# Optimization experiments

Measured on AMD Instinct MI355X. Metric: run time of the kernel, lower is better.

## Reference

```python
import jax, jax.numpy as jnp
import numpy as np

CHANNEL = 1
ALPHA = 1.0
EPS = 1e-10
SHAPE = (1, CHANNEL, 160, 192, 160)


def _sobel_kernels(channel):
    s2 = np.array([[-1., 0., 1.], [-2., 0., 2.], [-1., 0., 1.]], dtype=np.float32)
    # sobel.repeat(channel,1,3,1,1): 2D kernel tiled along depth -> k[d,h,w] = s2[h,w]
    kx = np.tile(s2[None, :, :], (3, 1, 1))
    ky = np.tile(s2.T[None, :, :], (3, 1, 1))
    kz = np.array([[[-1., -1., -1.], [-2., -2., -2.], [-1., -1., -1.]],
                   [[0., 0., 0.], [0., 0., 0.], [0., 0., 0.]],
                   [[1., 1., 1.], [2., 2., 2.], [1., 1., 1.]]], dtype=np.float32)
    def rep(k):  # -> [channel, 1, 3, 3, 3] for depthwise conv
        return jnp.asarray(np.tile(k[None, None], (channel, 1, 1, 1, 1)))
    return rep(kx), rep(ky), rep(kz)


def _conv3d(x, k, channel):
    # torch F.conv3d (cross-correlation), padding=1, groups=channel
    return jax.lax.conv_general_dilated(
        x, k, window_strides=(1, 1, 1), padding=((1, 1), (1, 1), (1, 1)),
        dimension_numbers=('NCDHW', 'OIDHW', 'NCDHW'),
        feature_group_count=channel)


def setup_inputs() -> dict:
    key = jax.random.key(0)
    k1, k2, k3 = jax.random.split(key, 3)
    M = jax.random.normal(k1, SHAPE, dtype=jnp.float32)
    S = jax.random.normal(k2, SHAPE, dtype=jnp.float32)
    flow = jax.random.normal(k3, (SHAPE[0], 3) + SHAPE[2:], dtype=jnp.float32)
    return {"M": M, "S": S, "flow": flow}


def reference(M, S, flow):
    kx, ky, kz = _sobel_kernels(CHANNEL)
    Idiff = M - S
    Sx = _conv3d(S, kx, CHANNEL)
    Sy = _conv3d(S, ky, CHANNEL)
    Sz = _conv3d(S, kz, CHANNEL)
    Mx = _conv3d(M, kx, CHANNEL)
    My = _conv3d(M, ky, CHANNEL)
    Mz = _conv3d(M, kz, CHANNEL)
    Sxyz_mag = Sx ** 2 + Sy ** 2 + Sz ** 2
    Mxyz_mag = Mx ** 2 + My ** 2 + Mz ** 2
    denom_S = Sxyz_mag + (ALPHA ** 2) * Idiff ** 2 + 1e-10
    denom_M = Mxyz_mag + (ALPHA ** 2) * Idiff ** 2 + 1e-10
    Ux = Idiff * (Sx / denom_S + Mx / denom_M)
    Uy = Idiff * (Sy / denom_S + My / denom_M)
    Uz = Idiff * (Sz / denom_S + Mz / denom_M)
    demons_ori_xz = jnp.arctan(Ux / (Uz + EPS))
    demons_ori_yz = jnp.arctan(Uy / (Uz + EPS))
    flow_ori_xz = jnp.arctan(flow[:, 0] / (flow[:, 2] + EPS))
    flow_ori_yz = jnp.arctan(flow[:, 1] / (flow[:, 2] + EPS))
    ori_error = jnp.mean((flow_ori_xz - demons_ori_xz) ** 2) + \
                jnp.mean((flow_ori_yz - demons_ori_yz) ** 2)
    return ori_error
```

## Files before the change

### kernel.cpp

```cpp
#include <hip/hip_runtime.h>
#include <math.h>

#define DD 160
#define HH 192
#define WW 160
#define TW 32
#define TH 8
#define TD 8
#define HW (HH * WW)
#define NVOX (DD * HH * WW)
#define HTW (TW + 2)
#define HTH (TH + 2)
#define HALO (HTW * HTH)

__device__ __forceinline__ float atan_fast(float r) {
    float ar = fabsf(r);
    float inv = __builtin_amdgcn_rcpf(ar);
    bool big = ar > 1.0f;
    float x = big ? inv : ar;
    float x2 = x * x;
    float p = fmaf(x2, fmaf(x2, fmaf(x2, fmaf(x2, fmaf(x2,
              -0.0117212f, 0.05265332f), -0.11643287f), 0.19354346f),
              -0.33262347f), 0.99997726f);
    p *= x;
    float res = big ? (1.57079632679489662f - p) : p;
    return copysignf(res, r);
}

__global__ __launch_bounds__(256) void demons_ori_kernel(
    const float* __restrict__ Mv, const float* __restrict__ Sv,
    const float* __restrict__ flow, float* __restrict__ out)
{
    __shared__ float buf[2][2][HTH][HTW];
    __shared__ float redbuf[4];

    const int tid = threadIdx.x;
    const int tw = tid & 31;
    const int th = tid >> 5;
    const int w0 = blockIdx.x * TW;
    const int h0 = blockIdx.y * TH;
    const int d0 = blockIdx.z * TD;

    int nst = 0;
    int sidx[2];
    int gbase[2];
    bool gok[2];
    for (int i = tid; i < HALO; i += 256) {
        int hh = i / HTW, ww = i - hh * HTW;
        int gh = h0 + hh - 1, gw = w0 + ww - 1;
        sidx[nst] = i;
        gok[nst] = (gh >= 0 && gh < HH && gw >= 0 && gw < WW);
        gbase[nst] = gh * WW + gw;
        nst++;
    }

    const int hc = th + 1, wc = tw + 1;

    auto stage = [&](int d, float pq[2][4]) {
        float* __restrict__ bS = &buf[d & 1][0][0][0];
        float* __restrict__ bM = &buf[d & 1][1][0][0];
        const bool din = (d >= 0) && (d < DD);
        for (int j = 0; j < nst; ++j) {
            float vs = 0.f, vm = 0.f;
            if (din && gok[j]) {
                size_t off = (size_t)d * HW + gbase[j];
                vs = Sv[off];
                vm = Mv[off];
            }
            bS[sidx[j]] = vs;
            bM[sidx[j]] = vm;
        }
        __syncthreads();
        #pragma unroll
        for (int f = 0; f < 2; ++f) {
            const float* __restrict__ b = f ? bM : bS;
            const float* r0 = b + (hc - 1) * HTW + (wc - 1);
            const float* r1 = r0 + HTW;
            const float* r2 = r1 + HTW;
            float v00 = r0[0], v01 = r0[1], v02 = r0[2];
            float v10 = r1[0], v11 = r1[1], v12 = r1[2];
            float v20 = r2[0], v21 = r2[1], v22 = r2[2];
            pq[f][0] = (v02 + 2.f * v12 + v22) - (v00 + 2.f * v10 + v20);
            pq[f][1] = (v20 + 2.f * v21 + v22) - (v00 + 2.f * v01 + v02);
            pq[f][2] = (v00 + v01 + v02) + 2.f * (v10 + v11 + v12)
                     + (v20 + v21 + v22);
            pq[f][3] = v11;
        }
    };

    float Pm[2][4], P0[2][4], Pp[2][4];
    stage(d0 - 1, Pm);
    stage(d0, P0);

    float lsum = 0.f;
    const size_t voff0 = (size_t)(h0 + th) * WW + (w0 + tw);

    #pragma unroll
    for (int dd = 0; dd < TD; ++dd) {
        const int d = d0 + dd;
        stage(d + 1, Pp);

        float idf = P0[1][3] - P0[0][3];
        float i2 = idf * idf + 1e-10f;
        float gxS = Pm[0][0] + P0[0][0] + Pp[0][0];
        float gyS = Pm[0][1] + P0[0][1] + Pp[0][1];
        float gzS = Pp[0][2] - Pm[0][2];
        float gxM = Pm[1][0] + P0[1][0] + Pp[1][0];
        float gyM = Pm[1][1] + P0[1][1] + Pp[1][1];
        float gzM = Pp[1][2] - Pm[1][2];
        float denS = gxS * gxS + gyS * gyS + gzS * gzS + i2;
        float denM = gxM * gxM + gyM * gyM + gzM * gzM + i2;
        float rS = __builtin_amdgcn_rcpf(denS);
        float rM = __builtin_amdgcn_rcpf(denM);
        float Ux = idf * (gxS * rS + gxM * rM);
        float Uy = idf * (gyS * rS + gyM * rM);
        float Uz = idf * (gzS * rS + gzM * rM);
        float rz = __builtin_amdgcn_rcpf(Uz + 1e-10f);
        float dxz = atan_fast(Ux * rz);
        float dyz = atan_fast(Uy * rz);

        size_t off = (size_t)d * HW + voff0;
        float f0 = flow[off];
        float f1 = flow[(size_t)NVOX + off];
        float f2 = flow[2 * (size_t)NVOX + off];
        float rf = __builtin_amdgcn_rcpf(f2 + 1e-10f);
        float fxz = atan_fast(f0 * rf);
        float fyz = atan_fast(f1 * rf);

        float e1 = fxz - dxz;
        float e2 = fyz - dyz;
        lsum += e1 * e1 + e2 * e2;

        #pragma unroll
        for (int f = 0; f < 2; ++f)
            #pragma unroll
            for (int q = 0; q < 4; ++q) {
                Pm[f][q] = P0[f][q];
                P0[f][q] = Pp[f][q];
            }
    }

    #pragma unroll
    for (int o = 32; o > 0; o >>= 1)
        lsum += __shfl_down(lsum, o, 64);
    if ((tid & 63) == 0)
        redbuf[tid >> 6] = lsum;
    __syncthreads();
    if (tid == 0) {
        float s = redbuf[0] + redbuf[1] + redbuf[2] + redbuf[3];
        atomicAdd(out, s * (1.0f / (float)NVOX));
    }
}

extern "C" void kernel_launch(void* const* d_in, const int* in_sizes, int n_in,
                              void* d_out, int out_size, void* d_ws, size_t ws_size,
                              hipStream_t stream) {
    const float* Mv   = (const float*)d_in[0];
    const float* Sv   = (const float*)d_in[1];
    const float* flow = (const float*)d_in[2];
    float* out = (float*)d_out;

    hipMemsetAsync(out, 0, sizeof(float), stream);

    dim3 grid(WW / TW, HH / TH, DD / TD);
    demons_ori_kernel<<<grid, dim3(256), 0, stream>>>(Mv, Sv, flow, out);
}
```

Baseline: 153.2 us.

## Prefetch depth slices into registers, compute two voxels per thread, cheaper atan

Each depth slice's global loads now go into registers one step ahead and are written to shared memory the next step, so global latency overlaps the stencil math. Each thread handles two adjacent W voxels using float2 shared-memory reads with a padded row stride, and the tile height doubles to 16. The flow components are loaded as float2 and prefetched one slice ahead, and launch bounds request 4 blocks per CU. The atan polynomial is replaced by a much lower-order approximation, which cuts ALU work but loses accuracy and may break tolerance.

```diff
diff --git a/kernel.cpp b/kernel.cpp
--- a/kernel.cpp
+++ b/kernel.cpp
@@ -5,139 +5,184 @@
 #define HH 192
 #define WW 160
 #define TW 32
-#define TH 8
+#define TH 16
 #define TD 8
 #define HW (HH * WW)
 #define NVOX (DD * HH * WW)
-#define HTW (TW + 2)
-#define HTH (TH + 2)
-#define HALO (HTW * HTH)
+#define HTW 34
+#define HTH 18
+#define HSTR 36
+#define HALO (HTH * HTW)
 
 __device__ __forceinline__ float atan_fast(float r) {
     float ar = fabsf(r);
+    bool big = ar > 1.0f;
     float inv = __builtin_amdgcn_rcpf(ar);
-    bool big = ar > 1.0f;
     float x = big ? inv : ar;
-    float x2 = x * x;
-    float p = fmaf(x2, fmaf(x2, fmaf(x2, fmaf(x2, fmaf(x2,
-              -0.0117212f, 0.05265332f), -0.11643287f), 0.19354346f),
-              -0.33262347f), 0.99997726f);
-    p *= x;
-    float res = big ? (1.57079632679489662f - p) : p;
+    float t = fmaf(0.0663f, x, 0.2447f);
+    float p = x * fmaf(1.0f - x, t, 0.78539816f);
+    float res = big ? (1.57079632679f - p) : p;
     return copysignf(res, r);
 }
 
-__global__ __launch_bounds__(256) void demons_ori_kernel(
+__global__ __launch_bounds__(256, 4) void demons_ori_kernel(
     const float* __restrict__ Mv, const float* __restrict__ Sv,
     const float* __restrict__ flow, float* __restrict__ out)
 {
-    __shared__ float buf[2][2][HTH][HTW];
+    __shared__ __attribute__((aligned(16))) float buf[2][2][HTH * HSTR];
     __shared__ float redbuf[4];
 
     const int tid = threadIdx.x;
-    const int tw = tid & 31;
-    const int th = tid >> 5;
+    const int twt = tid & 15;
+    const int th  = tid >> 4;
     const int w0 = blockIdx.x * TW;
     const int h0 = blockIdx.y * TH;
     const int d0 = blockIdx.z * TD;
 
     int nst = 0;
-    int sidx[2];
-    int gbase[2];
-    bool gok[2];
+    int sidx[3], gbase[3];
+    bool gok[3];
     for (int i = tid; i < HALO; i += 256) {
-        int hh = i / HTW, ww = i - hh * HTW;
+        int hh = i / HTW, ww = i - HTW * hh;
+        sidx[nst] = hh * HSTR + ww + 1;
         int gh = h0 + hh - 1, gw = w0 + ww - 1;
-        sidx[nst] = i;
         gok[nst] = (gh >= 0 && gh < HH && gw >= 0 && gw < WW);
         gbase[nst] = gh * WW + gw;
         nst++;
     }
 
-    const int hc = th + 1, wc = tw + 1;
-
-    auto stage = [&](int d, float pq[2][4]) {
-        float* __restrict__ bS = &buf[d & 1][0][0][0];
-        float* __restrict__ bM = &buf[d & 1][1][0][0];
+    float pfS[3], pfM[3];
+    auto issue = [&](int d) {
         const bool din = (d >= 0) && (d < DD);
-        for (int j = 0; j < nst; ++j) {
+        #pragma unroll
+        for (int j = 0; j < 3; ++j) {
             float vs = 0.f, vm = 0.f;
-            if (din && gok[j]) {
+            if (j < nst && din && gok[j]) {
                 size_t off = (size_t)d * HW + gbase[j];
                 vs = Sv[off];
                 vm = Mv[off];
             }
-            bS[sidx[j]] = vs;
-            bM[sidx[j]] = vm;
-        }
-        __syncthreads();
+            pfS[j] = vs; pfM[j] = vm;
+        }
+    };
+    auto commit = [&](int d) {
+        float* __restrict__ bS = &buf[d & 1][0][0];
+        float* __restrict__ bM = &buf[d & 1][1][0];
+        #pragma unroll
+        for (int j = 0; j < 3; ++j)
+            if (j < nst) { bS[sidx[j]] = pfS[j]; bM[sidx[j]] = pfM[j]; }
+    };
+
+    const int rbase = th * HSTR + 2 * twt;
+    auto partials = [&](int par, float pq[2][3][2], float ctr[2][2]) {
         #pragma unroll
         for (int f = 0; f < 2; ++f) {
-            const float* __restrict__ b = f ? bM : bS;
-            const float* r0 = b + (hc - 1) * HTW + (wc - 1);
-            const float* r1 = r0 + HTW;
-            const float* r2 = r1 + HTW;
-            float v00 = r0[0], v01 = r0[1], v02 = r0[2];
-            float v10 = r1[0], v11 = r1[1], v12 = r1[2];
-            float v20 = r2[0], v21 = r2[1], v22 = r2[2];
-            pq[f][0] = (v02 + 2.f * v12 + v22) - (v00 + 2.f * v10 + v20);
-            pq[f][1] = (v20 + 2.f * v21 + v22) - (v00 + 2.f * v01 + v02);
-            pq[f][2] = (v00 + v01 + v02) + 2.f * (v10 + v11 + v12)
-                     + (v20 + v21 + v22);
-            pq[f][3] = v11;
+            const float* __restrict__ b = &buf[par][f][0];
+            const float* r0 = b + rbase;
+            const float* r1 = r0 + HSTR;
+            const float* r2 = r1 + HSTR;
+            float2 A0 = *(const float2*)(r0);
+            float2 B0 = *(const float2*)(r0 + 2);
+            float2 C0 = *(const float2*)(r0 + 4);
+            float2 A1 = *(const float2*)(r1);
+            float2 B1 = *(const float2*)(r1 + 2);
+            float2 C1 = *(const float2*)(r1 + 4);
+            float2 A2 = *(const float2*)(r2);
+            float2 B2 = *(const float2*)(r2 + 2);
+            float2 C2 = *(const float2*)(r2 + 4);
+            float X0a = B0.y - A0.y, X0b = C0.x - B0.x;
+            float X1a = B1.y - A1.y, X1b = C1.x - B1.x;
+            float X2a = B2.y - A2.y, X2b = C2.x - B2.x;
+            float W0a = A0.y + 2.f * B0.x + B0.y, W0b = B0.x + 2.f * B0.y + C0.x;
+            float W2a = A2.y + 2.f * B2.x + B2.y, W2b = B2.x + 2.f * B2.y + C2.x;
+            float I0a = A0.y + B0.x + B0.y, I0b = B0.x + B0.y + C0.x;
+            float I1a = A1.y + B1.x + B1.y, I1b = B1.x + B1.y + C1.x;
+            float I2a = A2.y + B2.x + B2.y, I2b = B2.x + B2.y + C2.x;
+            pq[f][0][0] = X0a + 2.f * X1a + X2a;
+            pq[f][0][1] = X0b + 2.f * X1b + X2b;
+            pq[f][1][0] = W2a - W0a;
+            pq[f][1][1] = W2b - W0b;
+            pq[f][2][0] = I0a + 2.f * I1a + I2a;
+            pq[f][2][1] = I0b + 2.f * I1b + I2b;
+            ctr[f][0] = B1.x; ctr[f][1] = B1.y;
         }
     };
 
-    float Pm[2][4], P0[2][4], Pp[2][4];
-    stage(d0 - 1, Pm);
-    stage(d0, P0);
+    float Pm[2][3][2], P0[2][3][2], Pp[2][3][2];
+    float Cc[2][2], Cn[2][2], Cj[2][2];
+
+    issue(d0 - 1); commit(d0 - 1);
+    issue(d0);
+    __syncthreads();
+    partials((d0 - 1) & 1, Pm, Cj);
+    commit(d0);
+    issue(d0 + 1);
+    __syncthreads();
+    partials(d0 & 1, P0, Cc);
+
+    const size_t voff0 = (size_t)(h0 + th) * WW + (w0 + 2 * twt);
+    float2 Fx = *(const float2*)(flow + (size_t)d0 * HW + voff0);
+    float2 Fy = *(const float2*)(flow + (size_t)NVOX + (size_t)d0 * HW + voff0);
+    float2 Fz = *(const float2*)(flow + 2 * (size_t)NVOX + (size_t)d0 * HW + voff0);
 
     float lsum = 0.f;
-    const size_t voff0 = (size_t)(h0 + th) * WW + (w0 + tw);
 
     #pragma unroll
     for (int dd = 0; dd < TD; ++dd) {
         const int d = d0 + dd;
-        stage(d + 1, Pp);
-
-        float idf = P0[1][3] - P0[0][3];
-        float i2 = idf * idf + 1e-10f;
-        float gxS = Pm[0][0] + P0[0][0] + Pp[0][0];
-        float gyS = Pm[0][1] + P0[0][1] + Pp[0][1];
-        float gzS = Pp[0][2] - Pm[0][2];
-        float gxM = Pm[1][0] + P0[1][0] + Pp[1][0];
-        float gyM = Pm[1][1] + P0[1][1] + Pp[1][1];
-        float gzM = Pp[1][2] - Pm[1][2];
-        float denS = gxS * gxS + gyS * gyS + gzS * gzS + i2;
-        float denM = gxM * gxM + gyM * gyM + gzM * gzM + i2;
-        float rS = __builtin_amdgcn_rcpf(denS);
-        float rM = __builtin_amdgcn_rcpf(denM);
-        float Ux = idf * (gxS * rS + gxM * rM);
-        float Uy = idf * (gyS * rS + gyM * rM);
-        float Uz = idf * (gzS * rS + gzM * rM);
-        float rz = __builtin_amdgcn_rcpf(Uz + 1e-10f);
-        float dxz = atan_fast(Ux * rz);
-        float dyz = atan_fast(Uy * rz);
-
-        size_t off = (size_t)d * HW + voff0;
-        float f0 = flow[off];
-        float f1 = flow[(size_t)NVOX + off];
-        float f2 = flow[2 * (size_t)NVOX + off];
-        float rf = __builtin_amdgcn_rcpf(f2 + 1e-10f);
-        float fxz = atan_fast(f0 * rf);
-        float fyz = atan_fast(f1 * rf);
-
-        float e1 = fxz - dxz;
-        float e2 = fyz - dyz;
-        lsum += e1 * e1 + e2 * e2;
-
-        #pragma unroll
-        for (int f = 0; f < 2; ++f)
+        commit(d + 1);
+        float2 nFx, nFy, nFz;
+        if (dd < TD - 1) {
+            issue(d + 2);
+            size_t foff = (size_t)(d + 1) * HW + voff0;
+            nFx = *(const float2*)(flow + foff);
+            nFy = *(const float2*)(flow + (size_t)NVOX + foff);
+            nFz = *(const float2*)(flow + 2 * (size_t)NVOX + foff);
+        }
+        __syncthreads();
+        partials((d + 1) & 1, Pp, Cn);
+
+        #pragma unroll
+        for (int v = 0; v < 2; ++v) {
+            float idf = Cc[1][v] - Cc[0][v];
+            float i2 = idf * idf + 1e-10f;
+            float gxS = Pm[0][0][v] + P0[0][0][v] + Pp[0][0][v];
+            float gyS = Pm[0][1][v] + P0[0][1][v] + Pp[0][1][v];
+            float gzS = Pp[0][2][v] - Pm[0][2][v];
+            float gxM = Pm[1][0][v] + P0[1][0][v] + Pp[1][0][v];
+            float gyM = Pm[1][1][v] + P0[1][1][v] + Pp[1][1][v];
+            float gzM = Pp[1][2][v] - Pm[1][2][v];
+            float denS = gxS * gxS + gyS * gyS + gzS * gzS + i2;
+            float denM = gxM * gxM + gyM * gyM + gzM * gzM + i2;
+            float rS = __builtin_amdgcn_rcpf(denS);
+            float rM = __builtin_amdgcn_rcpf(denM);
+            float Ux = idf * (gxS * rS + gxM * rM);
+            float Uy = idf * (gyS * rS + gyM * rM);
+            float Uz = idf * (gzS * rS + gzM * rM);
+            float rz = __builtin_amdgcn_rcpf(Uz + 1e-10f);
+            float dxz = atan_fast(Ux * rz);
+            float dyz = atan_fast(Uy * rz);
+            float fx = v ? Fx.y : Fx.x;
+            float fy = v ? Fy.y : Fy.x;
+            float fz = v ? Fz.y : Fz.x;
+            float rf = __builtin_amdgcn_rcpf(fz + 1e-10f);
+            float fxz = atan_fast(fx * rf);
+            float fyz = atan_fast(fy * rf);
+            float e1 = fxz - dxz;
+            float e2 = fyz - dyz;
+            lsum += e1 * e1 + e2 * e2;
+        }
+
+        #pragma unroll
+        for (int f = 0; f < 2; ++f) {
             #pragma unroll
-            for (int q = 0; q < 4; ++q) {
-                Pm[f][q] = P0[f][q];
-                P0[f][q] = Pp[f][q];
+            for (int q = 0; q < 3; ++q) {
+                Pm[f][q][0] = P0[f][q][0]; Pm[f][q][1] = P0[f][q][1];
+                P0[f][q][0] = Pp[f][q][0]; P0[f][q][1] = Pp[f][q][1];
             }
+            Cc[f][0] = Cn[f][0]; Cc[f][1] = Cn[f][1];
+        }
+        if (dd < TD - 1) { Fx = nFx; Fy = nFy; Fz = nFz; }
     }
 
     #pragma unroll
```

New measurement: 252.8 us. 1.65x slower.

## Software-pipeline halo and flow loads one depth slice ahead of compute

Applied to the files above, without the earlier changes.

Splits the per-slice staging into issue (global loads into registers) and commit (store to shared memory). Loads for slice d+2 and the flow values for the next slice are now issued before the barrier and the stencil math of the current slice, so global memory latency overlaps with compute. This adds register pressure and reorders the barriers around the double-buffered shared tiles.

```diff
diff --git a/kernel.cpp b/kernel.cpp
--- a/kernel.cpp
+++ b/kernel.cpp
@@ -8,9 +8,9 @@
 #define TH 8
 #define TD 8
 #define HW (HH * WW)
-#define NVOX (DD * HH * WW)
-#define HTW (TW + 2)
-#define HTH (TH + 2)
+#define NVOX (DD * HW)
+#define HTW 34
+#define HTH 10
 #define HALO (HTW * HTH)
 
 __device__ __forceinline__ float atan_fast(float r) {
@@ -41,39 +41,49 @@
     const int h0 = blockIdx.y * TH;
     const int d0 = blockIdx.z * TD;
 
-    int nst = 0;
-    int sidx[2];
-    int gbase[2];
-    bool gok[2];
-    for (int i = tid; i < HALO; i += 256) {
-        int hh = i / HTW, ww = i - hh * HTW;
+    const bool has1 = (tid < HALO - 256);
+    int idx0, gb0, idx1 = 0, gb1 = 0;
+    bool ok0, ok1 = false;
+    {
+        int i = tid;
+        int hh = i / HTW, ww = i - HTW * hh;
         int gh = h0 + hh - 1, gw = w0 + ww - 1;
-        sidx[nst] = i;
-        gok[nst] = (gh >= 0 && gh < HH && gw >= 0 && gw < WW);
-        gbase[nst] = gh * WW + gw;
-        nst++;
+        idx0 = i;
+        ok0 = (gh >= 0 && gh < HH && gw >= 0 && gw < WW);
+        gb0 = gh * WW + gw;
+        if (has1) {
+            i = tid + 256;
+            hh = i / HTW; ww = i - HTW * hh;
+            gh = h0 + hh - 1; gw = w0 + ww - 1;
+            idx1 = i;
+            ok1 = (gh >= 0 && gh < HH && gw >= 0 && gw < WW);
+            gb1 = gh * WW + gw;
+        }
     }
 
-    const int hc = th + 1, wc = tw + 1;
+    float pS0 = 0.f, pM0 = 0.f, pS1 = 0.f, pM1 = 0.f;
 
-    auto stage = [&](int d, float pq[2][4]) {
+    auto issue = [&](int d) {
+        const bool din = (d >= 0) && (d < DD);
+        const size_t base = (size_t)d * HW;
+        pS0 = (din && ok0) ? Sv[base + gb0] : 0.f;
+        pM0 = (din && ok0) ? Mv[base + gb0] : 0.f;
+        pS1 = (din && ok1) ? Sv[base + gb1] : 0.f;
+        pM1 = (din && ok1) ? Mv[base + gb1] : 0.f;
+    };
+    auto commit = [&](int d) {
         float* __restrict__ bS = &buf[d & 1][0][0][0];
         float* __restrict__ bM = &buf[d & 1][1][0][0];
-        const bool din = (d >= 0) && (d < DD);
-        for (int j = 0; j < nst; ++j) {
-            float vs = 0.f, vm = 0.f;
-            if (din && gok[j]) {
-                size_t off = (size_t)d * HW + gbase[j];
-                vs = Sv[off];
-                vm = Mv[off];
-            }
-            bS[sidx[j]] = vs;
-            bM[sidx[j]] = vm;
-        }
-        __syncthreads();
+        bS[idx0] = pS0;
+        bM[idx0] = pM0;
+        if (has1) { bS[idx1] = pS1; bM[idx1] = pM1; }
+    };
+
+    const int hc = th + 1, wc = tw + 1;
+    auto partials = [&](int par, float pq[2][4]) {
         #pragma unroll
         for (int f = 0; f < 2; ++f) {
-            const float* __restrict__ b = f ? bM : bS;
+            const float* __restrict__ b = &buf[par][f][0][0];
             const float* r0 = b + (hc - 1) * HTW + (wc - 1);
             const float* r1 = r0 + HTW;
             const float* r2 = r1 + HTW;
@@ -89,16 +99,38 @@
     };
 
     float Pm[2][4], P0[2][4], Pp[2][4];
-    stage(d0 - 1, Pm);
-    stage(d0, P0);
+
+    issue(d0 - 1);
+    commit(d0 - 1);
+    issue(d0);
+    __syncthreads();
+    partials((d0 - 1) & 1, Pm);
+    commit(d0);
+    issue(d0 + 1);
+    __syncthreads();
+    partials(d0 & 1, P0);
+
+    const size_t voff0 = (size_t)(h0 + th) * WW + (w0 + tw);
+    float fFx = flow[(size_t)d0 * HW + voff0];
+    float fFy = flow[(size_t)NVOX + (size_t)d0 * HW + voff0];
+    float fFz = flow[2 * (size_t)NVOX + (size_t)d0 * HW + voff0];
 
     float lsum = 0.f;
-    const size_t voff0 = (size_t)(h0 + th) * WW + (w0 + tw);
 
     #pragma unroll
     for (int dd = 0; dd < TD; ++dd) {
         const int d = d0 + dd;
-        stage(d + 1, Pp);
+        commit(d + 1);
+        float nFx = 0.f, nFy = 0.f, nFz = 0.f;
+        if (dd < TD - 1) {
+            issue(d + 2);
+            size_t foff = (size_t)(d + 1) * HW + voff0;
+            nFx = flow[foff];
+            nFy = flow[(size_t)NVOX + foff];
+            nFz = flow[2 * (size_t)NVOX + foff];
+        }
+        __syncthreads();
+        partials((d + 1) & 1, Pp);
 
         float idf = P0[1][3] - P0[0][3];
         float i2 = idf * idf + 1e-10f;
@@ -119,13 +151,9 @@
         float dxz = atan_fast(Ux * rz);
         float dyz = atan_fast(Uy * rz);
 
-        size_t off = (size_t)d * HW + voff0;
-        float f0 = flow[off];
-        float f1 = flow[(size_t)NVOX + off];
-        float f2 = flow[2 * (size_t)NVOX + off];
-        float rf = __builtin_amdgcn_rcpf(f2 + 1e-10f);
-        float fxz = atan_fast(f0 * rf);
-        float fyz = atan_fast(f1 * rf);
+        float rf = __builtin_amdgcn_rcpf(fFz + 1e-10f);
+        float fxz = atan_fast(fFx * rf);
+        float fyz = atan_fast(fFy * rf);
 
         float e1 = fxz - dxz;
         float e2 = fyz - dyz;
@@ -138,6 +166,7 @@
                 Pm[f][q] = P0[f][q];
                 P0[f][q] = Pp[f][q];
             }
+        fFx = nFx; fFy = nFy; fFz = nFz;
     }
 
     #pragma unroll
```

Result: faster. 140.9 us (-8.1%).
